# Kernel tuning notes

Measured on AMD Instinct MI355X. Metric: run time of the kernel, lower is better.

Reference implementation:

```python
import jax, jax.numpy as jnp
import numpy as np

EPS = 1e-15

def setup_inputs() -> dict:
    key = jax.random.key(0)
    k1, k2, k3 = jax.random.split(key, 3)
    N, DIN, DOUT = 8192, 256, 256
    x = jax.random.normal(k1, (N, DIN), dtype=jnp.float32)
    A = jax.random.uniform(k2, (N, N), dtype=jnp.float32)
    W = jax.random.normal(k3, (DOUT, DIN), dtype=jnp.float32) * (1.0 / np.sqrt(DIN))
    return {"x": x, "A": A, "W": W}

def reference(x, A, W):
    # D = sign(relu(A - eps)) -> binary edge mask; deg_i = 1 + row sum
    mask = jnp.sign(jax.nn.relu(A - EPS))
    d = (1.0 + jnp.sum(mask, axis=1)) ** (-0.5)  # [N] diagonal of D
    N = A.shape[0]
    A_tilde = A + jnp.eye(N, dtype=A.dtype)       # A + I (square case)
    h = x @ W.T                                   # [N, DOUT] linear, no bias
    # diag(d) @ A_tilde @ diag(d) as row/col scaling (same math as diag matmuls)
    A_norm = d[:, None] * A_tilde * d[None, :]
    out = jax.nn.relu(A_norm @ h)
    return (out.astype(jnp.float32), A)
```

## Files before the change

### kernel.cpp

```cpp
#include <hip/hip_runtime.h>
#include <hip/hip_bf16.h>

constexpr int NN = 8192;
constexpr int DD = 256;

typedef __bf16 bf16_t;
typedef __bf16 bf16x8 __attribute__((ext_vector_type(8)));
typedef float  floatx4 __attribute__((ext_vector_type(4)));

#define GLOBAL_AS __attribute__((address_space(1)))
#define LDS_AS    __attribute__((address_space(3)))

__global__ __launch_bounds__(256) void k1_deg_copy(const float* __restrict__ A,
                                                   float* __restrict__ Aout,
                                                   float* __restrict__ dvec) {
    const int row = blockIdx.x;
    const int t = threadIdx.x;
    const floatx4* __restrict__ src = (const floatx4*)(A + (size_t)row * NN);
    floatx4* __restrict__ dst = (floatx4*)(Aout + (size_t)row * NN);
    int cnt = 0;
#pragma unroll
    for (int i = 0; i < 8; ++i) {
        floatx4 v = src[t + 256 * i];
        __builtin_nontemporal_store(v, &dst[t + 256 * i]);
        cnt += (v.x > 1e-15f) + (v.y > 1e-15f) + (v.z > 1e-15f) + (v.w > 1e-15f);
    }
#pragma unroll
    for (int off = 32; off > 0; off >>= 1) cnt += __shfl_down(cnt, off, 64);
    __shared__ int wsum[4];
    if ((t & 63) == 0) wsum[t >> 6] = cnt;
    __syncthreads();
    if (t == 0) {
        int total = wsum[0] + wsum[1] + wsum[2] + wsum[3];
        dvec[row] = rsqrtf(1.0f + (float)total);
    }
}

__device__ inline bf16x8 load_cvt8(const float* __restrict__ p) {
    floatx4 v0 = *(const floatx4*)p;
    floatx4 v1 = *(const floatx4*)(p + 4);
    bf16x8 r;
    r[0] = (bf16_t)v0.x; r[1] = (bf16_t)v0.y; r[2] = (bf16_t)v0.z; r[3] = (bf16_t)v0.w;
    r[4] = (bf16_t)v1.x; r[5] = (bf16_t)v1.y; r[6] = (bf16_t)v1.z; r[7] = (bf16_t)v1.w;
    return r;
}

__global__ __launch_bounds__(256) void k2_h_gt(const float* __restrict__ x,
                                               const float* __restrict__ W,
                                               const float* __restrict__ dvec,
                                               bf16_t* __restrict__ gT,
                                               float* __restrict__ out) {
    const int t = threadIdx.x;
    const int l = t & 63, w = t >> 6;
    const int lm = l & 15, q = l >> 4;
    const int nb = blockIdx.x & 3, jb = blockIdx.x >> 2;
    const int n0 = nb * 64 + w * 16;
    const int j0 = jb * 64;

    floatx4 acc[4] = {};
#pragma unroll
    for (int kt = 0; kt < 256; kt += 32) {
        const int k = kt + q * 8;
        bf16x8 a = load_cvt8(W + (size_t)(n0 + lm) * DD + k);
#pragma unroll
        for (int jt = 0; jt < 4; ++jt) {
            bf16x8 b = load_cvt8(x + (size_t)(j0 + jt * 16 + lm) * DD + k);
            acc[jt] = __builtin_amdgcn_mfma_f32_16x16x32_bf16(a, b, acc[jt], 0, 0, 0);
        }
    }
#pragma unroll
    for (int jt = 0; jt < 4; ++jt) {
        const int j = j0 + jt * 16 + lm;
        const float dj = dvec[j];
#pragma unroll
        for (int r = 0; r < 4; ++r) {
            const int n = n0 + q * 4 + r;
            const float hv = acc[jt][r];
            gT[(size_t)n * NN + j] = (bf16_t)(dj * hv);
            out[(size_t)j * DD + n] = dj * dj * hv;
        }
    }
}

__global__ __launch_bounds__(256, 3) void k3_gemm(const float* __restrict__ A,
                                                  const bf16_t* __restrict__ gT,
                                                  const float* __restrict__ dvec,
                                                  float* __restrict__ out) {
    __shared__ __align__(16) float As[2][64 * 64];
    __shared__ float sd[64];
    const int t = threadIdx.x;
    const int l = t & 63, w = t >> 6;
    const int lm = l & 15, q = l >> 4;
    const int mblk = blockIdx.x & 127, ks = blockIdx.x >> 7;
    const int m0 = mblk * 64;
    const int k0 = ks * 1024;

    if (t < 64) sd[t] = dvec[m0 + t];

    auto stage = [&](const float* Abase, int kc, float* buf) {
#pragma unroll
        for (int j = 0; j < 4; ++j) {
            const int p = j * 256 + t;
            const int m = p >> 4;
            const int klog = (p & 15) ^ (m & 15);
            const float* src = Abase + (size_t)(m0 + m) * NN + kc + klog * 4;
            float* ldsb = buf + (size_t)(j * 256 + w * 64) * 4;
            __builtin_amdgcn_global_load_lds((const GLOBAL_AS void*)src,
                                             (LDS_AS void*)ldsb, 16, 0, 0);
        }
    };
    auto read_a = [&](const float* buf, int m, int u0) -> bf16x8 {
        const int s = m & 15;
        const floatx4 f0 = *(const floatx4*)(buf + (size_t)(m * 16 + (u0 ^ s)) * 4);
        const floatx4 f1 = *(const floatx4*)(buf + (size_t)(m * 16 + ((u0 + 1) ^ s)) * 4);
        bf16x8 r;
        r[0] = (bf16_t)f0.x; r[1] = (bf16_t)f0.y; r[2] = (bf16_t)f0.z; r[3] = (bf16_t)f0.w;
        r[4] = (bf16_t)f1.x; r[5] = (bf16_t)f1.y; r[6] = (bf16_t)f1.z; r[7] = (bf16_t)f1.w;
        return r;
    };

    floatx4 acc[4][4] = {};
    const bf16_t* gb = gT + (size_t)(w * 64 + lm) * NN + k0 + q * 8;

    stage(A, k0, As[0]);
    __syncthreads();
    for (int c = 0; c < 16; ++c) {
        if (c + 1 < 16) stage(A, k0 + (c + 1) * 64, As[(c + 1) & 1]);
        const float* buf = As[c & 1];
#pragma unroll
        for (int kk = 0; kk < 64; kk += 32) {
            const size_t kg = (size_t)(c * 64 + kk);
            bf16x8 b0 = *(const bf16x8*)(gb + 0 * 16 * NN + kg);
            bf16x8 b1 = *(const bf16x8*)(gb + 1 * 16 * NN + kg);
            bf16x8 b2 = *(const bf16x8*)(gb + 2 * 16 * NN + kg);
            bf16x8 b3 = *(const bf16x8*)(gb + 3 * 16 * NN + kg);
            const int u0 = (kk >> 2) + 2 * q;
            bf16x8 a0 = read_a(buf, 0 * 16 + lm, u0);
            bf16x8 a1 = read_a(buf, 1 * 16 + lm, u0);
            bf16x8 a2 = read_a(buf, 2 * 16 + lm, u0);
            bf16x8 a3 = read_a(buf, 3 * 16 + lm, u0);
            acc[0][0] = __builtin_amdgcn_mfma_f32_16x16x32_bf16(a0, b0, acc[0][0], 0, 0, 0);
            acc[0][1] = __builtin_amdgcn_mfma_f32_16x16x32_bf16(a0, b1, acc[0][1], 0, 0, 0);
            acc[0][2] = __builtin_amdgcn_mfma_f32_16x16x32_bf16(a0, b2, acc[0][2], 0, 0, 0);
            acc[0][3] = __builtin_amdgcn_mfma_f32_16x16x32_bf16(a0, b3, acc[0][3], 0, 0, 0);
            acc[1][0] = __builtin_amdgcn_mfma_f32_16x16x32_bf16(a1, b0, acc[1][0], 0, 0, 0);
            acc[1][1] = __builtin_amdgcn_mfma_f32_16x16x32_bf16(a1, b1, acc[1][1], 0, 0, 0);
            acc[1][2] = __builtin_amdgcn_mfma_f32_16x16x32_bf16(a1, b2, acc[1][2], 0, 0, 0);
            acc[1][3] = __builtin_amdgcn_mfma_f32_16x16x32_bf16(a1, b3, acc[1][3], 0, 0, 0);
            acc[2][0] = __builtin_amdgcn_mfma_f32_16x16x32_bf16(a2, b0, acc[2][0], 0, 0, 0);
            acc[2][1] = __builtin_amdgcn_mfma_f32_16x16x32_bf16(a2, b1, acc[2][1], 0, 0, 0);
            acc[2][2] = __builtin_amdgcn_mfma_f32_16x16x32_bf16(a2, b2, acc[2][2], 0, 0, 0);
            acc[2][3] = __builtin_amdgcn_mfma_f32_16x16x32_bf16(a2, b3, acc[2][3], 0, 0, 0);
            acc[3][0] = __builtin_amdgcn_mfma_f32_16x16x32_bf16(a3, b0, acc[3][0], 0, 0, 0);
            acc[3][1] = __builtin_amdgcn_mfma_f32_16x16x32_bf16(a3, b1, acc[3][1], 0, 0, 0);
            acc[3][2] = __builtin_amdgcn_mfma_f32_16x16x32_bf16(a3, b2, acc[3][2], 0, 0, 0);
            acc[3][3] = __builtin_amdgcn_mfma_f32_16x16x32_bf16(a3, b3, acc[3][3], 0, 0, 0);
        }
        __syncthreads();
    }
#pragma unroll
    for (int mt = 0; mt < 4; ++mt)
#pragma unroll
        for (int r = 0; r < 4; ++r) {
            const int mrow = mt * 16 + q * 4 + r;
            const float dm = sd[mrow];
            const int m = m0 + mrow;
#pragma unroll
            for (int nt = 0; nt < 4; ++nt) {
                const int n = w * 64 + nt * 16 + lm;
                atomicAdd(out + (size_t)m * DD + n, dm * acc[mt][nt][r]);
            }
        }
}

__global__ __launch_bounds__(256) void k4_relu(float* __restrict__ out) {
    const int idx = blockIdx.x * 256 + threadIdx.x;
    floatx4* p = (floatx4*)out;
    floatx4 v = p[idx];
    v.x = fmaxf(v.x, 0.f); v.y = fmaxf(v.y, 0.f);
    v.z = fmaxf(v.z, 0.f); v.w = fmaxf(v.w, 0.f);
    p[idx] = v;
}

extern "C" void kernel_launch(void* const* d_in, const int* in_sizes, int n_in,
                              void* d_out, int out_size, void* d_ws, size_t ws_size,
                              hipStream_t stream) {
    const float* x = (const float*)d_in[0];
    const float* A = (const float*)d_in[1];
    const float* W = (const float*)d_in[2];
    float* out0 = (float*)d_out;
    float* out1 = out0 + (size_t)NN * DD;
    float* dvec = (float*)d_ws;
    bf16_t* gT = (bf16_t*)((char*)d_ws + 32768);

    k1_deg_copy<<<NN, 256, 0, stream>>>(A, out1, dvec);
    k2_h_gt<<<512, 256, 0, stream>>>(x, W, dvec, gT, out0);
    k3_gemm<<<1024, 256, 0, stream>>>(A, gT, dvec, out0);
    k4_relu<<<(NN * DD / 4) / 256, 256, 0, stream>>>(out0);
}
```

Measured before the change: 610.6 us.

## Drop split-K atomics, use 32x32 MFMA tiles and fuse ReLU into GEMM

The main GEMM now gives each block a full K range over a 32-row M tile and uses 32x32x16 MFMA instructions, instead of split-K over 64-row tiles with 16x16 MFMAs. This removes the atomic accumulation into the output and the separate ReLU kernel, since the epilogue adds the diagonal term, applies ReLU and stores directly. The cost is only 256 blocks doing long serial K loops, which lowers parallelism and occupancy on a GPU with many CUs. Each block also re-reads the full gT matrix.

```diff
diff --git a/kernel.cpp b/kernel.cpp
--- a/kernel.cpp
+++ b/kernel.cpp
@@ -6,7 +6,8 @@
 
 typedef __bf16 bf16_t;
 typedef __bf16 bf16x8 __attribute__((ext_vector_type(8)));
-typedef float  floatx4 __attribute__((ext_vector_type(4)));
+typedef float  floatx4  __attribute__((ext_vector_type(4)));
+typedef float  floatx16 __attribute__((ext_vector_type(16)));
 
 #define GLOBAL_AS __attribute__((address_space(1)))
 #define LDS_AS    __attribute__((address_space(3)))
@@ -82,104 +83,74 @@
     }
 }
 
-__global__ __launch_bounds__(256, 3) void k3_gemm(const float* __restrict__ A,
-                                                  const bf16_t* __restrict__ gT,
-                                                  const float* __restrict__ dvec,
-                                                  float* __restrict__ out) {
-    __shared__ __align__(16) float As[2][64 * 64];
-    __shared__ float sd[64];
+__global__ __launch_bounds__(256) void k3_gemm(const float* __restrict__ A,
+                                               const bf16_t* __restrict__ gT,
+                                               const float* __restrict__ dvec,
+                                               float* __restrict__ out) {
+    __shared__ __align__(16) float As[2][32 * 128];
+    __shared__ float sd[32];
     const int t = threadIdx.x;
     const int l = t & 63, w = t >> 6;
-    const int lm = l & 15, q = l >> 4;
-    const int mblk = blockIdx.x & 127, ks = blockIdx.x >> 7;
-    const int m0 = mblk * 64;
-    const int k0 = ks * 1024;
+    const int ln = l & 31, half = l >> 5;
+    const int m0 = blockIdx.x * 32;
 
-    if (t < 64) sd[t] = dvec[m0 + t];
+    if (t < 32) sd[t] = dvec[m0 + t];
 
-    auto stage = [&](const float* Abase, int kc, float* buf) {
+    auto stage = [&](int kc, float* buf) {
 #pragma unroll
         for (int j = 0; j < 4; ++j) {
             const int p = j * 256 + t;
-            const int m = p >> 4;
-            const int klog = (p & 15) ^ (m & 15);
-            const float* src = Abase + (size_t)(m0 + m) * NN + kc + klog * 4;
+            const int r = p >> 5;
+            const int ulog = (p & 31) ^ r;
+            const float* src = A + (size_t)(m0 + r) * NN + kc + ulog * 4;
             float* ldsb = buf + (size_t)(j * 256 + w * 64) * 4;
             __builtin_amdgcn_global_load_lds((const GLOBAL_AS void*)src,
                                              (LDS_AS void*)ldsb, 16, 0, 0);
         }
     };
-    auto read_a = [&](const float* buf, int m, int u0) -> bf16x8 {
-        const int s = m & 15;
-        const floatx4 f0 = *(const floatx4*)(buf + (size_t)(m * 16 + (u0 ^ s)) * 4);
-        const floatx4 f1 = *(const floatx4*)(buf + (size_t)(m * 16 + ((u0 + 1) ^ s)) * 4);
+    auto read_a = [&](const float* buf, int s) -> bf16x8 {
+        const int u0 = s * 4 + half * 2;
+        const floatx4 f0 = *(const floatx4*)(buf + (size_t)(ln * 32 + (u0 ^ ln)) * 4);
+        const floatx4 f1 = *(const floatx4*)(buf + (size_t)(ln * 32 + ((u0 + 1) ^ ln)) * 4);
         bf16x8 r;
         r[0] = (bf16_t)f0.x; r[1] = (bf16_t)f0.y; r[2] = (bf16_t)f0.z; r[3] = (bf16_t)f0.w;
         r[4] = (bf16_t)f1.x; r[5] = (bf16_t)f1.y; r[6] = (bf16_t)f1.z; r[7] = (bf16_t)f1.w;
         return r;
     };
 
-    floatx4 acc[4][4] = {};
-    const bf16_t* gb = gT + (size_t)(w * 64 + lm) * NN + k0 + q * 8;
+    floatx16 acc0 = {}, acc1 = {};
+    const bf16_t* gb = gT + (size_t)(w * 64 + ln) * NN + half * 8;
 
-    stage(A, k0, As[0]);
+    stage(0, As[0]);
     __syncthreads();
-    for (int c = 0; c < 16; ++c) {
-        if (c + 1 < 16) stage(A, k0 + (c + 1) * 64, As[(c + 1) & 1]);
+    for (int c = 0; c < 64; ++c) {
+        if (c + 1 < 64) stage((c + 1) * 128, As[(c + 1) & 1]);
         const float* buf = As[c & 1];
 #pragma unroll
-        for (int kk = 0; kk < 64; kk += 32) {
-            const size_t kg = (size_t)(c * 64 + kk);
-            bf16x8 b0 = *(const bf16x8*)(gb + 0 * 16 * NN + kg);
-            bf16x8 b1 = *(const bf16x8*)(gb + 1 * 16 * NN + kg);
-            bf16x8 b2 = *(const bf16x8*)(gb + 2 * 16 * NN + kg);
-            bf16x8 b3 = *(const bf16x8*)(gb + 3 * 16 * NN + kg);
-            const int u0 = (kk >> 2) + 2 * q;
-            bf16x8 a0 = read_a(buf, 0 * 16 + lm, u0);
-            bf16x8 a1 = read_a(buf, 1 * 16 + lm, u0);
-            bf16x8 a2 = read_a(buf, 2 * 16 + lm, u0);
-            bf16x8 a3 = read_a(buf, 3 * 16 + lm, u0);
-            acc[0][0] = __builtin_amdgcn_mfma_f32_16x16x32_bf16(a0, b0, acc[0][0], 0, 0, 0);
-            acc[0][1] = __builtin_amdgcn_mfma_f32_16x16x32_bf16(a0, b1, acc[0][1], 0, 0, 0);
-            acc[0][2] = __builtin_amdgcn_mfma_f32_16x16x32_bf16(a0, b2, acc[0][2], 0, 0, 0);
-            acc[0][3] = __builtin_amdgcn_mfma_f32_16x16x32_bf16(a0, b3, acc[0][3], 0, 0, 0);
-            acc[1][0] = __builtin_amdgcn_mfma_f32_16x16x32_bf16(a1, b0, acc[1][0], 0, 0, 0);
-            acc[1][1] = __builtin_amdgcn_mfma_f32_16x16x32_bf16(a1, b1, acc[1][1], 0, 0, 0);
-            acc[1][2] = __builtin_amdgcn_mfma_f32_16x16x32_bf16(a1, b2, acc[1][2], 0, 0, 0);
-            acc[1][3] = __builtin_amdgcn_mfma_f32_16x16x32_bf16(a1, b3, acc[1][3], 0, 0, 0);
-            acc[2][0] = __builtin_amdgcn_mfma_f32_16x16x32_bf16(a2, b0, acc[2][0], 0, 0, 0);
-            acc[2][1] = __builtin_amdgcn_mfma_f32_16x16x32_bf16(a2, b1, acc[2][1], 0, 0, 0);
-            acc[2][2] = __builtin_amdgcn_mfma_f32_16x16x32_bf16(a2, b2, acc[2][2], 0, 0, 0);
-            acc[2][3] = __builtin_amdgcn_mfma_f32_16x16x32_bf16(a2, b3, acc[2][3], 0, 0, 0);
-            acc[3][0] = __builtin_amdgcn_mfma_f32_16x16x32_bf16(a3, b0, acc[3][0], 0, 0, 0);
-            acc[3][1] = __builtin_amdgcn_mfma_f32_16x16x32_bf16(a3, b1, acc[3][1], 0, 0, 0);
-            acc[3][2] = __builtin_amdgcn_mfma_f32_16x16x32_bf16(a3, b2, acc[3][2], 0, 0, 0);
-            acc[3][3] = __builtin_amdgcn_mfma_f32_16x16x32_bf16(a3, b3, acc[3][3], 0, 0, 0);
+        for (int s = 0; s < 8; ++s) {
+            const size_t kg = (size_t)(c * 128 + s * 16);
+            bf16x8 a = read_a(buf, s);
+            bf16x8 b0 = *(const bf16x8*)(gb + kg);
+            bf16x8 b1 = *(const bf16x8*)(gb + (size_t)32 * NN + kg);
+            acc0 = __builtin_amdgcn_mfma_f32_32x32x16_bf16(a, b0, acc0, 0, 0, 0);
+            acc1 = __builtin_amdgcn_mfma_f32_32x32x16_bf16(a, b1, acc1, 0, 0, 0);
         }
         __syncthreads();
     }
+
 #pragma unroll
-    for (int mt = 0; mt < 4; ++mt)
+    for (int g = 0; g < 4; ++g)
 #pragma unroll
-        for (int r = 0; r < 4; ++r) {
-            const int mrow = mt * 16 + q * 4 + r;
-            const float dm = sd[mrow];
-            const int m = m0 + mrow;
-#pragma unroll
-            for (int nt = 0; nt < 4; ++nt) {
-                const int n = w * 64 + nt * 16 + lm;
-                atomicAdd(out + (size_t)m * DD + n, dm * acc[mt][nt][r]);
-            }
+        for (int r4 = 0; r4 < 4; ++r4) {
+            const int reg = g * 4 + r4;
+            const int ml = r4 + 8 * g + 4 * half;
+            const float dm = sd[ml];
+            float* p0 = out + (size_t)(m0 + ml) * DD + w * 64 + ln;
+            const float v0 = dm * acc0[reg] + p0[0];
+            const float v1 = dm * acc1[reg] + p0[32];
+            p0[0]  = fmaxf(v0, 0.f);
+            p0[32] = fmaxf(v1, 0.f);
         }
-}
-
-__global__ __launch_bounds__(256) void k4_relu(float* __restrict__ out) {
-    const int idx = blockIdx.x * 256 + threadIdx.x;
-    floatx4* p = (floatx4*)out;
-    floatx4 v = p[idx];
-    v.x = fmaxf(v.x, 0.f); v.y = fmaxf(v.y, 0.f);
-    v.z = fmaxf(v.z, 0.f); v.w = fmaxf(v.w, 0.f);
-    p[idx] = v;
 }
 
 extern "C" void kernel_launch(void* const* d_in, const int* in_sizes, int n_in,
@@ -195,6 +166,5 @@
 
     k1_deg_copy<<<NN, 256, 0, stream>>>(A, out1, dvec);
     k2_h_gt<<<512, 256, 0, stream>>>(x, W, dvec, gT, out0);
-    k3_gemm<<<1024, 256, 0, stream>>>(A, gT, dvec, out0);
-    k4_relu<<<(NN * DD / 4) / 256, 256, 0, stream>>>(out0);
+    k3_gemm<<<256, 256, 0, stream>>>(A, gT, dvec, out0);
 }
```

Measured after the change: 667.8 us. +9.4%, slower.
